# Optimization experiments

Measured on AMD Instinct MI355X. Metric: run time of the kernel, lower is better.

Reference implementation:

```python
import jax, jax.numpy as jnp
import numpy as np

R = 4            # search_range -> (2R+1)^2 = 81 displacement channels
B, C, H, W = 8, 128, 128, 224
CH_IN = C + (2 * R + 1) ** 2  # 209


def _conv2d(x, w, b):
    # x: [B,Cin,H,W], w: [Cout,Cin,3,3] -> SAME padding, stride 1
    y = jax.lax.conv_general_dilated(
        x, w, window_strides=(1, 1), padding='SAME',
        dimension_numbers=('NCHW', 'OIHW', 'NCHW'))
    return y + b[None, :, None, None]


def _leaky(x):
    return jnp.where(x >= 0, x, 0.1 * x)


def _correlation(x1, x2):
    # FlowNet-style correlation, kernel_size=1, stride1=stride2=1,
    # pad=max_displacement=R; normalized by number of elements (= C).
    b, c, h, w = x1.shape
    x2p = jnp.pad(x2, ((0, 0), (0, 0), (R, R), (R, R)))
    outs = []
    for dy in range(2 * R + 1):          # fixed 9x9 displacement window
        for dx in range(2 * R + 1):
            shifted = x2p[:, :, dy:dy + h, dx:dx + w]
            outs.append(jnp.mean(x1 * shifted, axis=1))  # [B,H,W]
    return jnp.stack(outs, axis=1)       # [B,81,H,W]


def _xavier_uniform(key, shape):
    fan_out = shape[0] * shape[2] * shape[3]
    fan_in = shape[1] * shape[2] * shape[3]
    a = jnp.sqrt(6.0 / (fan_in + fan_out))
    return jax.random.uniform(key, shape, jnp.float32, -a, a)


def setup_inputs() -> dict:
    key = jax.random.key(0)
    ks = jax.random.split(key, 10)
    return {
        'x1': jax.random.normal(ks[0], (B, C, H, W), jnp.float32),
        'x2': jax.random.normal(ks[1], (B, C, H, W), jnp.float32),
        'w1': _xavier_uniform(ks[2], (64, CH_IN, 3, 3)),
        'b1': jnp.zeros((64,), jnp.float32),
        'w2': _xavier_uniform(ks[3], (64, 64, 3, 3)),
        'b2': jnp.zeros((64,), jnp.float32),
        'w3': _xavier_uniform(ks[4], (32, 64, 3, 3)),
        'b3': jnp.zeros((32,), jnp.float32),
        'w4': _xavier_uniform(ks[5], (2, 32, 3, 3)),
        'b4': jnp.zeros((2,), jnp.float32),
    }


def reference(x1, x2, w1, b1, w2, b2, w3, b3, w4, b4):
    corr = _correlation(x1, x2)                 # [B,81,H,W]
    h = jnp.concatenate([x1, corr], axis=1)     # [B,209,H,W]
    h = _leaky(_conv2d(h, w1, b1))
    h = _leaky(_conv2d(h, w2, b2))
    h = _leaky(_conv2d(h, w3, b3))
    flow = _conv2d(h, w4, b4)                   # [B,2,H,W]
    return flow
```

## Files before the change

kernel.cpp:

```cpp
#include <hip/hip_runtime.h>
#include <hip/hip_bf16.h>
#include <cstddef>

#define BN 8
#define CCH 128
#define HH 128
#define WW 224
#define ND 81
#define CINP1 224

typedef __attribute__((ext_vector_type(8))) short short8_t;
typedef __attribute__((ext_vector_type(4))) float float4_t;

static __device__ __forceinline__ unsigned short f2bf(float f) {
  __hip_bfloat16 h = __float2bfloat16(f);
  return *(unsigned short*)&h;
}
static __device__ __forceinline__ float bf2f(short s) {
  unsigned u = ((unsigned)(unsigned short)s) << 16;
  return __uint_as_float(u);
}

__global__ __launch_bounds__(256) void convert_x1(
    const float* __restrict__ x1, uint4* __restrict__ a0q) {
  const int g = blockIdx.x * 256 + threadIdx.x;
  const int hw = HH * WW;
  const int b = g / hw, px = g - b * hw;
  const float* src = x1 + (size_t)b * CCH * hw + px;

  uint4 zero; zero.x = zero.y = zero.z = zero.w = 0u;
#pragma unroll
  for (int cq = 0; cq < 16; ++cq) {
    unsigned r[4];
#pragma unroll
    for (int j = 0; j < 4; ++j) {
      const int c = cq * 8 + j * 2;
      const float f0 = src[(size_t)(c + 0) * hw];
      const float f1 = src[(size_t)(c + 1) * hw];
      r[j] = (unsigned)f2bf(f0) | ((unsigned)f2bf(f1) << 16);
    }
    uint4 u; u.x = r[0]; u.y = r[1]; u.z = r[2]; u.w = r[3];
    a0q[(size_t)g * 28 + cq] = u;
  }
  a0q[(size_t)g * 28 + 26] = zero;
  a0q[(size_t)g * 28 + 27] = zero;
}

__global__ __launch_bounds__(512, 2) void corr_mfma(
    const float* __restrict__ x2,
    const uint4* __restrict__ a0q,
    __hip_bfloat16* __restrict__ a0) {
  __shared__ uint4 sB[4 * 576];
  const int tid = threadIdx.x;
  const int lane = tid & 63, w = tid >> 6;
  const int m = lane & 15, q = lane >> 4;
  const int x0 = blockIdx.x * 16, y0 = blockIdx.y * 16, b = blockIdx.z;
  const int hw = HH * WW;

  float4_t acc[2][9][2];
#pragma unroll
  for (int yy = 0; yy < 2; ++yy)
#pragma unroll
    for (int d = 0; d < 9; ++d)
#pragma unroll
      for (int t = 0; t < 2; ++t) acc[yy][d][t] = (float4_t)0.0f;

  for (int cb = 0; cb < 4; ++cb) {
    __syncthreads();
    for (int s = tid; s < 2304; s += 512) {
      const int qs = s / 576, rc = s - qs * 576;
      const int r = rc / 24, c = rc - r * 24;
      const int gy = y0 - 4 + r, gx = x0 - 4 + c;
      uint4 u; u.x = u.y = u.z = u.w = 0u;
      if (gy >= 0 && gy < HH && gx >= 0 && gx < WW) {
        const float* p2 =
            x2 + (size_t)(b * CCH + cb * 32 + qs * 8) * hw + gy * WW + gx;
        unsigned rr[4];
#pragma unroll
        for (int j = 0; j < 4; ++j) {
          const float f0 = p2[(size_t)(2 * j + 0) * hw];
          const float f1 = p2[(size_t)(2 * j + 1) * hw];
          rr[j] = (unsigned)f2bf(f0) | ((unsigned)f2bf(f1) << 16);
        }
        u.x = rr[0]; u.y = rr[1]; u.z = rr[2]; u.w = rr[3];
      }
      sB[s] = u;
    }
    __syncthreads();

    uint4 afr[2];
#pragma unroll
    for (int yy = 0; yy < 2; ++yy) {
      const int y = y0 + 2 * w + yy;
      afr[yy] = a0q[((size_t)(b * HH + y) * WW + x0 + m) * 28 + cb * 4 + q];
    }

#pragma unroll
    for (int yy = 0; yy < 2; ++yy) {
      const short8_t af = *(const short8_t*)&afr[yy];
#pragma unroll
      for (int dyi = 0; dyi < 9; ++dyi) {
        const int r = 2 * w + yy + dyi;
#pragma unroll
        for (int t = 0; t < 2; ++t) {
          const short8_t bf =
              *(const short8_t*)&sB[q * 576 + r * 24 + 8 * t + m];
          acc[yy][dyi][t] = __builtin_amdgcn_mfma_f32_16x16x32_bf16(
              af, bf, acc[yy][dyi][t], 0, 0, 0);
        }
      }
    }
  }

  const float sc = 1.0f / 128.0f;
#pragma unroll
  for (int yy = 0; yy < 2; ++yy) {
    const int y = y0 + 2 * w + yy;
    __hip_bfloat16* dst = a0 + ((size_t)(b * HH + y) * WW + x0) * CINP1;
#pragma unroll
    for (int dyi = 0; dyi < 9; ++dyi) {
#pragma unroll
      for (int t = 0; t < 2; ++t) {
#pragma unroll
        for (int r = 0; r < 4; ++r) {
          const int mm = 4 * q + r;
          const int nabs = 8 * t + m;
          const int dxi = nabs - mm;
          if (dxi >= 0 && dxi <= 8 && (t == 0 || m >= 8)) {
            dst[(size_t)mm * CINP1 + 128 + dyi * 9 + dxi] =
                __float2bfloat16(acc[yy][dyi][t][r] * sc);
          }
        }
      }
    }
  }
}

__global__ void repack_w_bf16(const float* __restrict__ w,
                              __hip_bfloat16* __restrict__ wt,
                              int COUT, int CIN, int CINPAD) {
  const int idx = blockIdx.x * 256 + threadIdx.x;
  const int n = 9 * COUT * CINPAD;
  if (idx >= n) return;
  const int t = idx / (COUT * CINPAD);
  const int rem = idx - t * (COUT * CINPAD);
  const int co = rem / CINPAD;
  const int ci = rem - co * CINPAD;
  const float v = (ci < CIN) ? w[(size_t)(co * CIN + ci) * 9 + t] : 0.0f;
  wt[idx] = __float2bfloat16(v);
}

template <int CINPAD, int COUT, bool LEAKY>
__global__ __launch_bounds__(256, 2) void conv_mfma(
    const uint4* __restrict__ inq,
    const __hip_bfloat16* __restrict__ wt,
    const float* __restrict__ bias,
    __hip_bfloat16* __restrict__ out) {
  constexpr int NT = COUT / 16;
  constexpr int NCB = CINPAD / 32;
  constexpr int QSTRIDE_A = 324;
  __shared__ uint4 sA[4 * QSTRIDE_A];
  __shared__ uint4 sW[4 * 9 * COUT];

  const int tid = threadIdx.x;
  const int lane = tid & 63, w = tid >> 6;
  const int m = lane & 15, q = lane >> 4;
  const int x0 = blockIdx.x * 16, y0 = blockIdx.y * 16, b = blockIdx.z;
  const uint4* wq = (const uint4*)wt;

  float4_t acc[4][NT];
#pragma unroll
  for (int my = 0; my < 4; ++my)
#pragma unroll
    for (int nt = 0; nt < NT; ++nt) acc[my][nt] = (float4_t)0.0f;

  for (int cb = 0; cb < NCB; ++cb) {
    __syncthreads();
    for (int s = tid; s < 324; s += 256) {
      const int pr = s / 18, pc = s - pr * 18;
      const int gy = y0 - 1 + pr, gx = x0 - 1 + pc;
      uint4 c0, c1, c2, c3;
      if (gy >= 0 && gy < HH && gx >= 0 && gx < WW) {
        const size_t base =
            ((size_t)(b * HH + gy) * WW + gx) * (CINPAD / 8) + cb * 4;
        c0 = inq[base + 0]; c1 = inq[base + 1];
        c2 = inq[base + 2]; c3 = inq[base + 3];
      } else {
        c0.x=c0.y=c0.z=c0.w=0u; c1=c0; c2=c0; c3=c0;
      }
      sA[0 * QSTRIDE_A + s] = c0;
      sA[1 * QSTRIDE_A + s] = c1;
      sA[2 * QSTRIDE_A + s] = c2;
      sA[3 * QSTRIDE_A + s] = c3;
    }
    for (int s = tid; s < 9 * COUT; s += 256) {
      const int t = s / COUT, co = s - t * COUT;
      const size_t base = ((size_t)(t * COUT + co) * CINPAD + cb * 32) / 8;
      const uint4 c0 = wq[base + 0], c1 = wq[base + 1];
      const uint4 c2 = wq[base + 2], c3 = wq[base + 3];
      sW[(0 * 9 + t) * COUT + co] = c0;
      sW[(1 * 9 + t) * COUT + co] = c1;
      sW[(2 * 9 + t) * COUT + co] = c2;
      sW[(3 * 9 + t) * COUT + co] = c3;
    }
    __syncthreads();

#pragma unroll
    for (int t = 0; t < 9; ++t) {
      const int dy = t / 3 - 1, dx = t % 3 - 1;
      short8_t bf[NT];
#pragma unroll
      for (int nt = 0; nt < NT; ++nt) {
        bf[nt] = *(const short8_t*)&sW[(q * 9 + t) * COUT + nt * 16 + m];
      }
#pragma unroll
      for (int my = 0; my < 4; ++my) {
        const int row = 4 * w + my + dy + 1;
        const int col = m + dx + 1;
        const short8_t af =
            *(const short8_t*)&sA[q * QSTRIDE_A + row * 18 + col];
#pragma unroll
        for (int nt = 0; nt < NT; ++nt) {
          acc[my][nt] = __builtin_amdgcn_mfma_f32_16x16x32_bf16(
              af, bf[nt], acc[my][nt], 0, 0, 0);
        }
      }
    }
  }

#pragma unroll
  for (int my = 0; my < 4; ++my) {
    const int y = y0 + 4 * w + my;
#pragma unroll
    for (int nt = 0; nt < NT; ++nt) {
      const int co = nt * 16 + m;
      const float bv = bias[co];
#pragma unroll
      for (int r = 0; r < 4; ++r) {
        const int x = x0 + q * 4 + r;
        float v = acc[my][nt][r] + bv;
        if (LEAKY) v = (v >= 0.0f) ? v : 0.1f * v;
        out[((size_t)(b * HH + y) * WW + x) * COUT + co] = __float2bfloat16(v);
      }
    }
  }
}

__global__ __launch_bounds__(256, 2) void conv4_kernel(
    const uint4* __restrict__ inq,
    const __hip_bfloat16* __restrict__ wt,
    const float* __restrict__ bias,
    float* __restrict__ out) {
  __shared__ uint4 sA[4 * 324];
  __shared__ uint4 sW[9 * 2 * 4];
  const int tid = threadIdx.x;
  const int tx = tid & 15, ty = tid >> 4;
  const int x0 = blockIdx.x * 16, y0 = blockIdx.y * 16, b = blockIdx.z;

  for (int s = tid; s < 324; s += 256) {
    const int pr = s / 18, pc = s - pr * 18;
    const int gy = y0 - 1 + pr, gx = x0 - 1 + pc;
    uint4 c0, c1, c2, c3;
    if (gy >= 0 && gy < HH && gx >= 0 && gx < WW) {
      const size_t base = ((size_t)(b * HH + gy) * WW + gx) * 4;
      c0 = inq[base + 0]; c1 = inq[base + 1];
      c2 = inq[base + 2]; c3 = inq[base + 3];
    } else {
      c0.x=c0.y=c0.z=c0.w=0u; c1=c0; c2=c0; c3=c0;
    }
    sA[0 * 324 + s] = c0; sA[1 * 324 + s] = c1;
    sA[2 * 324 + s] = c2; sA[3 * 324 + s] = c3;
  }
  if (tid < 72) sW[tid] = ((const uint4*)wt)[tid];
  __syncthreads();

  float acc0 = bias[0], acc1 = bias[1];
#pragma unroll
  for (int t = 0; t < 9; ++t) {
    const int dy = t / 3 - 1, dx = t % 3 - 1;
    const int row = ty + dy + 1, col = tx + dx + 1;
#pragma unroll
    for (int qi = 0; qi < 4; ++qi) {
      const short8_t a = *(const short8_t*)&sA[qi * 324 + row * 18 + col];
      const short8_t w0 = *(const short8_t*)&sW[(t * 2 + 0) * 4 + qi];
      const short8_t w1 = *(const short8_t*)&sW[(t * 2 + 1) * 4 + qi];
#pragma unroll
      for (int j = 0; j < 8; ++j) {
        const float av = bf2f(a[j]);
        acc0 += av * bf2f(w0[j]);
        acc1 += av * bf2f(w1[j]);
      }
    }
  }
  const int y = y0 + ty, x = x0 + tx;
  out[((size_t)(b * 2 + 0) * HH + y) * WW + x] = acc0;
  out[((size_t)(b * 2 + 1) * HH + y) * WW + x] = acc1;
}

extern "C" void kernel_launch(void* const* d_in, const int* in_sizes, int n_in,
                              void* d_out, int out_size, void* d_ws,
                              size_t ws_size, hipStream_t stream) {
  const float* x1 = (const float*)d_in[0];
  const float* x2 = (const float*)d_in[1];
  const float* w1 = (const float*)d_in[2];
  const float* b1 = (const float*)d_in[3];
  const float* w2 = (const float*)d_in[4];
  const float* b2 = (const float*)d_in[5];
  const float* w3 = (const float*)d_in[6];
  const float* b3 = (const float*)d_in[7];
  const float* w4 = (const float*)d_in[8];
  const float* b4 = (const float*)d_in[9];
  float* out = (float*)d_out;

  char* ws = (char*)d_ws;
  __hip_bfloat16* A0 = (__hip_bfloat16*)ws;
  const size_t A0_BYTES = (size_t)BN * HH * WW * CINP1 * 2;
  __hip_bfloat16* h1 = (__hip_bfloat16*)(ws + A0_BYTES);
  const size_t H1_BYTES = (size_t)BN * HH * WW * 64 * 2;
  __hip_bfloat16* wt1 = (__hip_bfloat16*)(ws + A0_BYTES + H1_BYTES);
  __hip_bfloat16* wt2 = wt1 + 9 * 64 * CINP1;
  __hip_bfloat16* wt3 = wt2 + 9 * 64 * 64;
  __hip_bfloat16* wt4 = wt3 + 9 * 32 * 64;
  __hip_bfloat16* h2 = (__hip_bfloat16*)ws;
  __hip_bfloat16* h3 = (__hip_bfloat16*)(ws + H1_BYTES);

  {
    int n1 = 9 * 64 * CINP1;
    repack_w_bf16<<<(n1 + 255) / 256, 256, 0, stream>>>(w1, wt1, 64, 209, CINP1);
    int n2 = 9 * 64 * 64;
    repack_w_bf16<<<(n2 + 255) / 256, 256, 0, stream>>>(w2, wt2, 64, 64, 64);
    int n3 = 9 * 32 * 64;
    repack_w_bf16<<<(n3 + 255) / 256, 256, 0, stream>>>(w3, wt3, 32, 64, 64);
    int n4 = 9 * 2 * 32;
    repack_w_bf16<<<(n4 + 255) / 256, 256, 0, stream>>>(w4, wt4, 2, 32, 32);
  }

  convert_x1<<<BN * HH * WW / 256, 256, 0, stream>>>(x1, (uint4*)A0);

  corr_mfma<<<dim3(WW / 16, HH / 16, BN), dim3(512), 0, stream>>>(
      x2, (const uint4*)A0, A0);

  const dim3 grid(WW / 16, HH / 16, BN);
  conv_mfma<CINP1, 64, true>
      <<<grid, 256, 0, stream>>>((const uint4*)A0, wt1, b1, h1);
  conv_mfma<64, 64, true>
      <<<grid, 256, 0, stream>>>((const uint4*)h1, wt2, b2, h2);
  conv_mfma<64, 32, true>
      <<<grid, 256, 0, stream>>>((const uint4*)h2, wt3, b3, h3);
  conv4_kernel<<<grid, 256, 0, stream>>>((const uint4*)h3, wt4, b4, out);
}
```

Measured before the change: 537.5 us.

## Vectorize x2 staging loads and reuse LDS fragments in correlation and conv kernels

The correlation kernel now loads x2 as float4 along x, with a scalar fallback at the borders, and writes four packed bf16 LDS entries per thread instead of doing scalar gathers. Its MFMA loop walks the 10 shared rows once, so each B fragment loaded from LDS feeds both output rows. The conv kernel preloads its 6x3 A fragments from LDS into registers once per channel block, so they are not reloaded for every one of the 9 taps. The aim is fewer global and LDS load instructions, paid for with higher register pressure from the 18 uint4 fragments plus the accumulators, which could lower occupancy.

```diff
diff --git a/kernel.cpp b/kernel.cpp
--- a/kernel.cpp
+++ b/kernel.cpp
@@ -67,24 +67,39 @@
 
   for (int cb = 0; cb < 4; ++cb) {
     __syncthreads();
-    for (int s = tid; s < 2304; s += 512) {
-      const int qs = s / 576, rc = s - qs * 576;
-      const int r = rc / 24, c = rc - r * 24;
-      const int gy = y0 - 4 + r, gx = x0 - 4 + c;
-      uint4 u; u.x = u.y = u.z = u.w = 0u;
-      if (gy >= 0 && gy < HH && gx >= 0 && gx < WW) {
-        const float* p2 =
-            x2 + (size_t)(b * CCH + cb * 32 + qs * 8) * hw + gy * WW + gx;
-        unsigned rr[4];
-#pragma unroll
-        for (int j = 0; j < 4; ++j) {
-          const float f0 = p2[(size_t)(2 * j + 0) * hw];
-          const float f1 = p2[(size_t)(2 * j + 1) * hw];
-          rr[j] = (unsigned)f2bf(f0) | ((unsigned)f2bf(f1) << 16);
+    for (int s = tid; s < 576; s += 512) {
+      const int qs = s / 144, rc = s - qs * 144;
+      const int r = rc / 6, c4 = rc - r * 6;
+      const int gy = y0 - 4 + r, gx = x0 - 4 + c4 * 4;
+      const float* p2 = x2 + (size_t)(b * CCH + cb * 32 + qs * 8) * hw;
+      float va[4][8];
+      if (gy >= 0 && gy < HH && gx >= 0 && gx + 3 < WW) {
+#pragma unroll
+        for (int e = 0; e < 8; ++e) {
+          const float4 v = *(const float4*)&p2[(size_t)e * hw + gy * WW + gx];
+          va[0][e] = v.x; va[1][e] = v.y; va[2][e] = v.z; va[3][e] = v.w;
         }
-        u.x = rr[0]; u.y = rr[1]; u.z = rr[2]; u.w = rr[3];
-      }
-      sB[s] = u;
+      } else {
+#pragma unroll
+        for (int e = 0; e < 8; ++e) {
+          const float* pe = p2 + (size_t)e * hw;
+#pragma unroll
+          for (int j = 0; j < 4; ++j) {
+            const int xx = gx + j;
+            va[j][e] = (gy >= 0 && gy < HH && xx >= 0 && xx < WW)
+                           ? pe[gy * WW + xx] : 0.0f;
+          }
+        }
+      }
+#pragma unroll
+      for (int j = 0; j < 4; ++j) {
+        uint4 u;
+        u.x = (unsigned)f2bf(va[j][0]) | ((unsigned)f2bf(va[j][1]) << 16);
+        u.y = (unsigned)f2bf(va[j][2]) | ((unsigned)f2bf(va[j][3]) << 16);
+        u.z = (unsigned)f2bf(va[j][4]) | ((unsigned)f2bf(va[j][5]) << 16);
+        u.w = (unsigned)f2bf(va[j][6]) | ((unsigned)f2bf(va[j][7]) << 16);
+        sB[qs * 576 + r * 24 + c4 * 4 + j] = u;
+      }
     }
     __syncthreads();
 
@@ -94,20 +109,25 @@
       const int y = y0 + 2 * w + yy;
       afr[yy] = a0q[((size_t)(b * HH + y) * WW + x0 + m) * 28 + cb * 4 + q];
     }
-
-#pragma unroll
-    for (int yy = 0; yy < 2; ++yy) {
-      const short8_t af = *(const short8_t*)&afr[yy];
-#pragma unroll
-      for (int dyi = 0; dyi < 9; ++dyi) {
-        const int r = 2 * w + yy + dyi;
-#pragma unroll
-        for (int t = 0; t < 2; ++t) {
-          const short8_t bf =
-              *(const short8_t*)&sB[q * 576 + r * 24 + 8 * t + m];
-          acc[yy][dyi][t] = __builtin_amdgcn_mfma_f32_16x16x32_bf16(
-              af, bf, acc[yy][dyi][t], 0, 0, 0);
-        }
+    const short8_t af0 = *(const short8_t*)&afr[0];
+    const short8_t af1 = *(const short8_t*)&afr[1];
+
+#pragma unroll
+    for (int rr = 0; rr < 10; ++rr) {
+      const int r = 2 * w + rr;
+      const short8_t bf0 = *(const short8_t*)&sB[q * 576 + r * 24 + m];
+      const short8_t bf1 = *(const short8_t*)&sB[q * 576 + r * 24 + 8 + m];
+      if (rr <= 8) {
+        acc[0][rr][0] = __builtin_amdgcn_mfma_f32_16x16x32_bf16(
+            af0, bf0, acc[0][rr][0], 0, 0, 0);
+        acc[0][rr][1] = __builtin_amdgcn_mfma_f32_16x16x32_bf16(
+            af0, bf1, acc[0][rr][1], 0, 0, 0);
+      }
+      if (rr >= 1) {
+        acc[1][rr - 1][0] = __builtin_amdgcn_mfma_f32_16x16x32_bf16(
+            af1, bf0, acc[1][rr - 1][0], 0, 0, 0);
+        acc[1][rr - 1][1] = __builtin_amdgcn_mfma_f32_16x16x32_bf16(
+            af1, bf1, acc[1][rr - 1][1], 0, 0, 0);
       }
     }
   }
@@ -205,9 +225,17 @@
     }
     __syncthreads();
 
+    uint4 afr[6][3];
+#pragma unroll
+    for (int pr6 = 0; pr6 < 6; ++pr6)
+#pragma unroll
+      for (int ds = 0; ds < 3; ++ds)
+        afr[pr6][ds] =
+            sA[q * QSTRIDE_A + (4 * w + pr6) * 18 + m + ds];
+
 #pragma unroll
     for (int t = 0; t < 9; ++t) {
-      const int dy = t / 3 - 1, dx = t % 3 - 1;
+      const int tr = t / 3, ds = t % 3;
       short8_t bf[NT];
 #pragma unroll
       for (int nt = 0; nt < NT; ++nt) {
@@ -215,10 +243,7 @@
       }
 #pragma unroll
       for (int my = 0; my < 4; ++my) {
-        const int row = 4 * w + my + dy + 1;
-        const int col = m + dx + 1;
-        const short8_t af =
-            *(const short8_t*)&sA[q * QSTRIDE_A + row * 18 + col];
+        const short8_t af = *(const short8_t*)&afr[my + tr][ds];
 #pragma unroll
         for (int nt = 0; nt < NT; ++nt) {
           acc[my][nt] = __builtin_amdgcn_mfma_f32_16x16x32_bf16(
```

New measurement: 551.3 us. +2.6%, slower.

## Double-buffer conv input tiles, read weights from global, reuse corr B-fragments

Applied to the files above, without the earlier changes.

In the conv kernels the input halo tile is now double-buffered in shared memory, so the next channel block is loaded while the current one is computed, and one barrier per iteration is removed. Weights are repacked into a fragment-friendly layout and read straight from global/L2 instead of being staged in LDS. That frees shared memory and allows an occupancy hint of 3 blocks per CU instead of 2. The correlation kernel reuses each loaded B fragment across the two output rows, roughly halving its LDS reads. The cost is more global weight traffic per wave and added register pressure under the tighter launch bound.

```diff
diff --git a/kernel.cpp b/kernel.cpp
--- a/kernel.cpp
+++ b/kernel.cpp
@@ -94,20 +94,25 @@
       const int y = y0 + 2 * w + yy;
       afr[yy] = a0q[((size_t)(b * HH + y) * WW + x0 + m) * 28 + cb * 4 + q];
     }
-
-#pragma unroll
-    for (int yy = 0; yy < 2; ++yy) {
-      const short8_t af = *(const short8_t*)&afr[yy];
-#pragma unroll
-      for (int dyi = 0; dyi < 9; ++dyi) {
-        const int r = 2 * w + yy + dyi;
-#pragma unroll
-        for (int t = 0; t < 2; ++t) {
-          const short8_t bf =
-              *(const short8_t*)&sB[q * 576 + r * 24 + 8 * t + m];
-          acc[yy][dyi][t] = __builtin_amdgcn_mfma_f32_16x16x32_bf16(
-              af, bf, acc[yy][dyi][t], 0, 0, 0);
-        }
+    const short8_t af0 = *(const short8_t*)&afr[0];
+    const short8_t af1 = *(const short8_t*)&afr[1];
+
+#pragma unroll
+    for (int rr = 0; rr < 10; ++rr) {
+      const int r = 2 * w + rr;
+      const short8_t bf0 = *(const short8_t*)&sB[q * 576 + r * 24 + m];
+      const short8_t bf1 = *(const short8_t*)&sB[q * 576 + r * 24 + 8 + m];
+      if (rr <= 8) {
+        acc[0][rr][0] = __builtin_amdgcn_mfma_f32_16x16x32_bf16(
+            af0, bf0, acc[0][rr][0], 0, 0, 0);
+        acc[0][rr][1] = __builtin_amdgcn_mfma_f32_16x16x32_bf16(
+            af0, bf1, acc[0][rr][1], 0, 0, 0);
+      }
+      if (rr >= 1) {
+        acc[1][rr - 1][0] = __builtin_amdgcn_mfma_f32_16x16x32_bf16(
+            af1, bf0, acc[1][rr - 1][0], 0, 0, 0);
+        acc[1][rr - 1][1] = __builtin_amdgcn_mfma_f32_16x16x32_bf16(
+            af1, bf1, acc[1][rr - 1][1], 0, 0, 0);
       }
     }
   }
@@ -134,6 +139,23 @@
       }
     }
   }
+}
+
+__global__ void repack_w_q(const float* __restrict__ w,
+                           __hip_bfloat16* __restrict__ wt,
+                           int COUT, int CIN, int CINPAD) {
+  const int idx = blockIdx.x * 256 + threadIdx.x;
+  const int n = 9 * COUT * CINPAD;
+  if (idx >= n) return;
+  const int e = idx & 7;
+  int r = idx >> 3;
+  const int co = r % COUT; r /= COUT;
+  const int qq = r & 3;    r >>= 2;
+  const int t = r % 9;     r /= 9;
+  const int cb = r;
+  const int ci = cb * 32 + qq * 8 + e;
+  const float v = (ci < CIN) ? w[(size_t)(co * CIN + ci) * 9 + t] : 0.0f;
+  wt[idx] = __float2bfloat16(v);
 }
 
 __global__ void repack_w_bf16(const float* __restrict__ w,
@@ -151,22 +173,19 @@
 }
 
 template <int CINPAD, int COUT, bool LEAKY>
-__global__ __launch_bounds__(256, 2) void conv_mfma(
+__global__ __launch_bounds__(256, 3) void conv_mfma(
     const uint4* __restrict__ inq,
-    const __hip_bfloat16* __restrict__ wt,
+    const uint4* __restrict__ wq,
     const float* __restrict__ bias,
     __hip_bfloat16* __restrict__ out) {
   constexpr int NT = COUT / 16;
   constexpr int NCB = CINPAD / 32;
-  constexpr int QSTRIDE_A = 324;
-  __shared__ uint4 sA[4 * QSTRIDE_A];
-  __shared__ uint4 sW[4 * 9 * COUT];
+  __shared__ uint4 sA[2 * 4 * 324];
 
   const int tid = threadIdx.x;
   const int lane = tid & 63, w = tid >> 6;
   const int m = lane & 15, q = lane >> 4;
   const int x0 = blockIdx.x * 16, y0 = blockIdx.y * 16, b = blockIdx.z;
-  const uint4* wq = (const uint4*)wt;
 
   float4_t acc[4][NT];
 #pragma unroll
@@ -174,8 +193,7 @@
 #pragma unroll
     for (int nt = 0; nt < NT; ++nt) acc[my][nt] = (float4_t)0.0f;
 
-  for (int cb = 0; cb < NCB; ++cb) {
-    __syncthreads();
+  auto stage = [&](int cb, int half) {
     for (int s = tid; s < 324; s += 256) {
       const int pr = s / 18, pc = s - pr * 18;
       const int gy = y0 - 1 + pr, gx = x0 - 1 + pc;
@@ -186,39 +204,35 @@
         c0 = inq[base + 0]; c1 = inq[base + 1];
         c2 = inq[base + 2]; c3 = inq[base + 3];
       } else {
-        c0.x=c0.y=c0.z=c0.w=0u; c1=c0; c2=c0; c3=c0;
-      }
-      sA[0 * QSTRIDE_A + s] = c0;
-      sA[1 * QSTRIDE_A + s] = c1;
-      sA[2 * QSTRIDE_A + s] = c2;
-      sA[3 * QSTRIDE_A + s] = c3;
-    }
-    for (int s = tid; s < 9 * COUT; s += 256) {
-      const int t = s / COUT, co = s - t * COUT;
-      const size_t base = ((size_t)(t * COUT + co) * CINPAD + cb * 32) / 8;
-      const uint4 c0 = wq[base + 0], c1 = wq[base + 1];
-      const uint4 c2 = wq[base + 2], c3 = wq[base + 3];
-      sW[(0 * 9 + t) * COUT + co] = c0;
-      sW[(1 * 9 + t) * COUT + co] = c1;
-      sW[(2 * 9 + t) * COUT + co] = c2;
-      sW[(3 * 9 + t) * COUT + co] = c3;
-    }
+        c0.x = c0.y = c0.z = c0.w = 0u; c1 = c0; c2 = c0; c3 = c0;
+      }
+      sA[(half * 4 + 0) * 324 + s] = c0;
+      sA[(half * 4 + 1) * 324 + s] = c1;
+      sA[(half * 4 + 2) * 324 + s] = c2;
+      sA[(half * 4 + 3) * 324 + s] = c3;
+    }
+  };
+
+  stage(0, 0);
+  for (int cb = 0; cb < NCB; ++cb) {
     __syncthreads();
+    if (cb + 1 < NCB) stage(cb + 1, (cb + 1) & 1);
+    const int half = cb & 1;
 
 #pragma unroll
     for (int t = 0; t < 9; ++t) {
-      const int dy = t / 3 - 1, dx = t % 3 - 1;
+      const int tr = t / 3, ds = t % 3;
+      const uint4* wbase = wq + (size_t)((cb * 9 + t) * 4 + q) * COUT;
       short8_t bf[NT];
 #pragma unroll
       for (int nt = 0; nt < NT; ++nt) {
-        bf[nt] = *(const short8_t*)&sW[(q * 9 + t) * COUT + nt * 16 + m];
+        bf[nt] = *(const short8_t*)&wbase[nt * 16 + m];
       }
 #pragma unroll
       for (int my = 0; my < 4; ++my) {
-        const int row = 4 * w + my + dy + 1;
-        const int col = m + dx + 1;
+        const int row = 4 * w + my + tr;
         const short8_t af =
-            *(const short8_t*)&sA[q * QSTRIDE_A + row * 18 + col];
+            *(const short8_t*)&sA[(half * 4 + q) * 324 + row * 18 + m + ds];
 #pragma unroll
         for (int nt = 0; nt < NT; ++nt) {
           acc[my][nt] = __builtin_amdgcn_mfma_f32_16x16x32_bf16(
@@ -326,11 +340,11 @@
 
   {
     int n1 = 9 * 64 * CINP1;
-    repack_w_bf16<<<(n1 + 255) / 256, 256, 0, stream>>>(w1, wt1, 64, 209, CINP1);
+    repack_w_q<<<(n1 + 255) / 256, 256, 0, stream>>>(w1, wt1, 64, 209, CINP1);
     int n2 = 9 * 64 * 64;
-    repack_w_bf16<<<(n2 + 255) / 256, 256, 0, stream>>>(w2, wt2, 64, 64, 64);
+    repack_w_q<<<(n2 + 255) / 256, 256, 0, stream>>>(w2, wt2, 64, 64, 64);
     int n3 = 9 * 32 * 64;
-    repack_w_bf16<<<(n3 + 255) / 256, 256, 0, stream>>>(w3, wt3, 32, 64, 64);
+    repack_w_q<<<(n3 + 255) / 256, 256, 0, stream>>>(w3, wt3, 32, 64, 64);
     int n4 = 9 * 2 * 32;
     repack_w_bf16<<<(n4 + 255) / 256, 256, 0, stream>>>(w4, wt4, 2, 32, 32);
   }
@@ -342,10 +356,10 @@
 
   const dim3 grid(WW / 16, HH / 16, BN);
   conv_mfma<CINP1, 64, true>
-      <<<grid, 256, 0, stream>>>((const uint4*)A0, wt1, b1, h1);
+      <<<grid, 256, 0, stream>>>((const uint4*)A0, (const uint4*)wt1, b1, h1);
   conv_mfma<64, 64, true>
-      <<<grid, 256, 0, stream>>>((const uint4*)h1, wt2, b2, h2);
+      <<<grid, 256, 0, stream>>>((const uint4*)h1, (const uint4*)wt2, b2, h2);
   conv_mfma<64, 32, true>
-      <<<grid, 256, 0, stream>>>((const uint4*)h2, wt3, b3, h3);
+      <<<grid, 256, 0, stream>>>((const uint4*)h2, (const uint4*)wt3, b3, h3);
   conv4_kernel<<<grid, 256, 0, stream>>>((const uint4*)h3, wt4, b4, out);
 }
```

Measured after the change: 564.2 us. 1.05x slower.
